# Performance work log

Measured on AMD Instinct MI355X. Metric: run time of the kernel, lower is better.

## Reference

```python
import jax, jax.numpy as jnp
import numpy as np

B, S, D, H = 4, 2048, 1024, 16
HD = D // H  # head size = 64


def setup_inputs() -> dict:
    key = jax.random.key(0)
    ks = jax.random.split(key, 5)
    x = jax.random.normal(ks[0], (B, S, D), dtype=jnp.float32)
    scale = 1.0 / np.sqrt(D)
    Wq = jax.random.normal(ks[1], (H, D, HD), dtype=jnp.float32) * scale
    Wk = jax.random.normal(ks[2], (H, D, HD), dtype=jnp.float32) * scale
    Wv = jax.random.normal(ks[3], (H, D, HD), dtype=jnp.float32) * scale
    W_O = jax.random.normal(ks[4], (D, D), dtype=jnp.float32) * scale
    return {"x": x, "Wq": Wq, "Wk": Wk, "Wv": Wv, "W_O": W_O}


def reference(x, Wq, Wk, Wv, W_O):
    # Per-head Q/K/V projections, batched across heads via einsum.
    q = jnp.einsum("bsd,hde->bhse", x, Wq)  # [B,H,S,HD]
    k = jnp.einsum("bsd,hde->bhse", x, Wk)
    v = jnp.einsum("bsd,hde->bhse", x, Wv)
    scores = jnp.einsum("bhse,bhte->bhst", q, k) / jnp.sqrt(
        jnp.asarray(HD, dtype=x.dtype)
    )  # [B,H,S,S]
    # Causal mask (GPT-style attention head).
    causal = jnp.tril(jnp.ones((S, S), dtype=bool))
    scores = jnp.where(causal, scores, jnp.finfo(scores.dtype).min)
    attn = jax.nn.softmax(scores, axis=-1)
    out = jnp.einsum("bhst,bhte->bhse", attn, v)  # [B,H,S,HD]
    # Concat heads: [B,S,H,HD] -> [B,S,D]
    concat = out.transpose(0, 2, 1, 3).reshape(B, S, D)
    # nn.Linear(D, D, bias=False): y = x @ W_O^T
    return concat @ W_O.T
```

## Files before the change

### kernel.cpp

```cpp
#include <hip/hip_runtime.h>
#include <hip/hip_bf16.h>

#define BB 4
#define SS 2048
#define DD 1024
#define HH 16
#define HDD 64

typedef __attribute__((ext_vector_type(8))) short bf16x8;
typedef __attribute__((ext_vector_type(8))) unsigned short u16x8;
typedef __attribute__((ext_vector_type(4))) float f32x4;
typedef __attribute__((ext_vector_type(4))) unsigned int u32x4;

#define GLD_LDS16(g, l) \
    __builtin_amdgcn_global_load_lds((const __attribute__((address_space(1))) void*)(g), \
                                     (__attribute__((address_space(3))) void*)(l), 16, 0, 0)

__device__ __forceinline__ unsigned short f32_to_bf16(float f) {
    unsigned int u = __float_as_uint(f);
    u += 0x7fffu + ((u >> 16) & 1u);
    return (unsigned short)(u >> 16);
}

__device__ __forceinline__ unsigned int cvt_pk_bf16(float lo, float hi) {
    unsigned int r;
    asm("v_cvt_pk_bf16_f32 %0, %1, %2" : "=v"(r) : "v"(lo), "v"(hi));
    return r;
}

__global__ __launch_bounds__(256) void prep(
    const float* __restrict__ x, const float* __restrict__ Wq,
    const float* __restrict__ Wk, const float* __restrict__ Wv,
    const float* __restrict__ WO, unsigned short* __restrict__ xb,
    unsigned short* __restrict__ wob, unsigned short* __restrict__ wqkvT) {
    __shared__ float tile[64][68];
    int bid = blockIdx.x, t = threadIdx.x;
    if (bid < 2048) {
        for (int i = bid * 256 + t; i < 2097152; i += 2048 * 256) {
            float4 v = ((const float4*)x)[i];
            ushort4 o;
            o.x = f32_to_bf16(v.x); o.y = f32_to_bf16(v.y);
            o.z = f32_to_bf16(v.z); o.w = f32_to_bf16(v.w);
            ((ushort4*)xb)[i] = o;
        }
    } else if (bid < 2304) {
        for (int i = (bid - 2048) * 256 + t; i < 262144; i += 256 * 256) {
            float4 v = ((const float4*)WO)[i];
            ushort4 o;
            o.x = f32_to_bf16(v.x); o.y = f32_to_bf16(v.y);
            o.z = f32_to_bf16(v.z); o.w = f32_to_bf16(v.w);
            ((ushort4*)wob)[i] = o;
        }
    } else {
        int b2 = bid - 2304;
        int w = b2 >> 8, h = (b2 >> 4) & 15, db = b2 & 15;
        const float* src = (w == 0) ? Wq : ((w == 1) ? Wk : Wv);
        for (int p = t; p < 1024; p += 256) {
            int row = p >> 4, c4 = p & 15;
            float4 v = *(const float4*)(src + ((size_t)(h * 1024 + db * 64 + row)) * 64 + c4 * 4);
            tile[row][c4 * 4 + 0] = v.x; tile[row][c4 * 4 + 1] = v.y;
            tile[row][c4 * 4 + 2] = v.z; tile[row][c4 * 4 + 3] = v.w;
        }
        __syncthreads();
        size_t wbase = (size_t)w * 1024 * 1024;
        for (int p = t; p < 512; p += 256) {
            int e = p >> 3, c = p & 7;
            u16x8 pk;
#pragma unroll
            for (int j = 0; j < 8; ++j) pk[j] = f32_to_bf16(tile[c * 8 + j][e]);
            *(u16x8*)(wqkvT + wbase + (size_t)(h * 64 + e) * 1024 + db * 64 + c * 8) = pk;
        }
    }
}

template <int EPI>
__global__ __launch_bounds__(256) void gemm128(
    const unsigned short* __restrict__ A, const unsigned short* __restrict__ Bm,
    void* __restrict__ C0, void* __restrict__ C1, void* __restrict__ C2, int NBt) {
    __shared__ unsigned short sh[2][128 * 64];
    int cpx = gridDim.x >> 3;
    int bid = (blockIdx.x & 7) * cpx + (blockIdx.x >> 3);
    int mb = bid / NBt, nb = bid % NBt;
    int tid = threadIdx.x;
    int lane = tid & 63, wid = tid >> 6;
    int wm = wid >> 1, wn = wid & 1;
    int g = lane >> 4, lr = lane & 15;
    int srow = lane >> 3, sch = lane & 7;
    int scol = (sch ^ srow) * 8;
    const int M0 = mb * 128, N0 = nb * 128;

    f32x4 acc[4][4] = {};

    for (int kt = 0; kt < 16; ++kt) {
        __syncthreads();
#pragma unroll
        for (int i = 0; i < 4; ++i) {
            int c = wid * 4 + i;
            int row = c * 8 + srow;
            GLD_LDS16(A + (size_t)(M0 + row) * 1024 + kt * 64 + scol, &sh[0][c * 512]);
            GLD_LDS16(Bm + (size_t)(N0 + row) * 1024 + kt * 64 + scol, &sh[1][c * 512]);
        }
        __syncthreads();
#pragma unroll
        for (int kk = 0; kk < 2; ++kk) {
            bf16x8 af[4], bfr[4];
#pragma unroll
            for (int i = 0; i < 4; ++i) {
                int row = wm * 64 + i * 16 + lr;
                int ch = (kk * 4 + g) ^ (row & 7);
                af[i] = *(const bf16x8*)&sh[0][row * 64 + ch * 8];
                int rowb = wn * 64 + i * 16 + lr;
                int chb = (kk * 4 + g) ^ (rowb & 7);
                bfr[i] = *(const bf16x8*)&sh[1][rowb * 64 + chb * 8];
            }
            __builtin_amdgcn_s_setprio(1);
#pragma unroll
            for (int i = 0; i < 4; ++i)
#pragma unroll
                for (int j = 0; j < 4; ++j)
                    acc[i][j] = __builtin_amdgcn_mfma_f32_16x16x32_bf16(af[i], bfr[j], acc[i][j], 0, 0, 0);
            __builtin_amdgcn_s_setprio(0);
        }
    }

    if constexpr (EPI == 0) {
        unsigned short (*T)[128] = (unsigned short(*)[128])sh;
        if (nb < 16) {
            unsigned short* dst0 = (nb < 8) ? (unsigned short*)C0 : (unsigned short*)C1;
            const float QSCALE = 0.125f * 1.4426950408889634f;
            float scl = (nb < 8) ? QSCALE : 1.0f;
            __syncthreads();
#pragma unroll
            for (int i = 0; i < 4; ++i)
#pragma unroll
                for (int j = 0; j < 4; ++j)
#pragma unroll
                    for (int r = 0; r < 4; ++r) {
                        int ml = wm * 64 + i * 16 + g * 4 + r;
                        int nl = wn * 64 + j * 16 + lr;
                        T[ml][nl ^ ((ml & 7) << 3)] = f32_to_bf16(acc[i][j][r] * scl);
                    }
            __syncthreads();
            int b = M0 >> 11, s0 = M0 & 2047;
            int h0 = (N0 >> 6) & 15;
#pragma unroll
            for (int itr = 0; itr < 8; ++itr) {
                int idx = itr * 256 + tid;
                int row = idx >> 4, seg = idx & 15;
                u16x8 vv = *(const u16x8*)&T[row][(seg * 8) ^ ((row & 7) << 3)];
                int h = h0 + (seg >> 3), e0 = (seg & 7) * 8;
                *(u16x8*)(dst0 + ((size_t)(b * HH + h) * SS + s0 + row) * HDD + e0) = vv;
            }
        } else {
            __syncthreads();
#pragma unroll
            for (int i = 0; i < 4; ++i)
#pragma unroll
                for (int j = 0; j < 4; ++j)
#pragma unroll
                    for (int r = 0; r < 4; ++r) {
                        int nl = wn * 64 + j * 16 + lr;
                        int ml = wm * 64 + i * 16 + g * 4 + r;
                        T[nl][ml ^ ((nl & 7) << 3)] = f32_to_bf16(acc[i][j][r]);
                    }
            __syncthreads();
            unsigned short* Vo = (unsigned short*)C2;
            int b = M0 >> 11, s0 = M0 & 2047;
            int nb16 = nb - 16;
#pragma unroll
            for (int itr = 0; itr < 8; ++itr) {
                int idx = itr * 256 + tid;
                int row = idx >> 4, seg = idx & 15;
                u16x8 vv = *(const u16x8*)&T[row][(seg * 8) ^ ((row & 7) << 3)];
                int h = (nb16 * 128 + row) >> 6;
                int e = row & 63;
                *(u16x8*)(Vo + (((size_t)(b * HH + h)) * HDD + e) * SS + s0 + seg * 8) = vv;
            }
        }
    } else {
        float* Co = (float*)C0;
#pragma unroll
        for (int i = 0; i < 4; ++i)
#pragma unroll
            for (int j = 0; j < 4; ++j)
#pragma unroll
                for (int r = 0; r < 4; ++r) {
                    int m = M0 + wm * 64 + i * 16 + g * 4 + r;
                    int n = N0 + wn * 64 + j * 16 + lr;
                    Co[(size_t)m * 1024 + n] = acc[i][j][r];
                }
    }
}

__global__ __launch_bounds__(256, 4) void attn_fwd(
    const unsigned short* __restrict__ Q, const unsigned short* __restrict__ K,
    const unsigned short* __restrict__ VT, unsigned short* __restrict__ O) {
    int bid = blockIdx.x;
    int qb = 15 - (bid >> 6);
    int bh = bid & 63;
    int b = bh >> 4, h = bh & 15;
    int tid = threadIdx.x, lane = tid & 63, w = tid >> 6;
    int g = lane >> 4, lr = lane & 15;
    int srow = lane >> 3, sch = lane & 7;
    int scol = (sch ^ srow) * 8;

    __shared__ unsigned short smem[16384];

    const int q0 = qb * 128;
    const unsigned short* Qp = Q + ((size_t)bh * SS + q0 + w * 32) * HDD;
    const unsigned short* Kp = K + (size_t)bh * SS * HDD;
    const unsigned short* Vp = VT + (size_t)bh * HDD * SS;

    bf16x8 qf[2][2];
#pragma unroll
    for (int qg = 0; qg < 2; ++qg) {
        qf[qg][0] = *(const bf16x8*)(Qp + (qg * 16 + lr) * 64 + g * 8);
        qf[qg][1] = *(const bf16x8*)(Qp + (qg * 16 + lr) * 64 + 32 + g * 8);
    }

    bf16x8 ones;
#pragma unroll
    for (int i = 0; i < 8; ++i) ones[i] = (short)0x3F80;

    f32x4 acc[2][4] = {};
    f32x4 acc_l[2] = {};

    const int nt = 2 * qb + 2;

#pragma unroll
    for (int i = 0; i < 2; ++i) {
        int c = w * 2 + i;
        int row = c * 8 + srow;
        GLD_LDS16(Kp + (size_t)row * HDD + scol, smem + c * 512);
        GLD_LDS16(Vp + (size_t)row * SS + scol, smem + 8192 + c * 512);
    }
    __syncthreads();

    auto tile_body = [&](int it, unsigned short* Kcur, unsigned short* Vcur,
                         unsigned short* Knxt, unsigned short* Vnxt, bool stage) {
        if (stage) {
            int t1 = (it + 1) * 64;
#pragma unroll
            for (int i = 0; i < 2; ++i) {
                int c = w * 2 + i;
                int row = c * 8 + srow;
                GLD_LDS16(Kp + (size_t)(t1 + row) * HDD + scol, Knxt + c * 512);
                GLD_LDS16(Vp + (size_t)row * SS + t1 + scol, Vnxt + c * 512);
            }
        }
        int t0 = it * 64;

        f32x4 sacc[2][4] = {};
        __builtin_amdgcn_s_setprio(1);
#pragma unroll
        for (int kk = 0; kk < 2; ++kk)
#pragma unroll
            for (int ct = 0; ct < 4; ++ct) {
                int row = ct * 16 + lr;
                int ch = (kk * 4 + g) ^ (row & 7);
                bf16x8 kf = *(const bf16x8*)(Kcur + row * 64 + ch * 8);
#pragma unroll
                for (int qg = 0; qg < 2; ++qg)
                    sacc[qg][ct] = __builtin_amdgcn_mfma_f32_16x16x32_bf16(kf, qf[qg][kk], sacc[qg][ct], 0, 0, 0);
            }
        __builtin_amdgcn_s_setprio(0);

        if (it >= nt - 2) {
#pragma unroll
            for (int qg = 0; qg < 2; ++qg) {
                int kmax = q0 + w * 32 + qg * 16 + lr - t0;
#pragma unroll
                for (int ct = 0; ct < 4; ++ct)
#pragma unroll
                    for (int r = 0; r < 4; ++r)
                        if (ct * 16 + g * 4 + r > kmax) sacc[qg][ct][r] = -3.0e38f;
            }
        }

        bf16x8 pvf[2][2];
#pragma unroll
        for (int qg = 0; qg < 2; ++qg) {
            unsigned int pk[4][2];
#pragma unroll
            for (int ct = 0; ct < 4; ++ct) {
                float p0 = exp2f(sacc[qg][ct][0]);
                float p1 = exp2f(sacc[qg][ct][1]);
                float p2 = exp2f(sacc[qg][ct][2]);
                float p3 = exp2f(sacc[qg][ct][3]);
                pk[ct][0] = cvt_pk_bf16(p0, p1);
                pk[ct][1] = cvt_pk_bf16(p2, p3);
            }
            unsigned int out[2][4];
#pragma unroll
            for (int s5 = 0; s5 < 2; ++s5)
#pragma unroll
                for (int s1 = 0; s1 < 2; ++s1) {
                    unsigned int a = pk[2 * s5][s1];
                    unsigned int bq = pk[2 * s5 + 1][s1];
                    asm("v_permlane32_swap_b32 %0, %1" : "+v"(a), "+v"(bq));
                    asm("v_permlane16_swap_b32 %0, %1" : "+v"(a), "+v"(bq));
                    out[s5][s1] = a;
                    out[s5][2 + s1] = bq;
                }
#pragma unroll
            for (int kk2 = 0; kk2 < 2; ++kk2) {
                u32x4 tmp;
                tmp[0] = out[kk2][0]; tmp[1] = out[kk2][1];
                tmp[2] = out[kk2][2]; tmp[3] = out[kk2][3];
                pvf[qg][kk2] = __builtin_bit_cast(bf16x8, tmp);
            }
#pragma unroll
            for (int kk2 = 0; kk2 < 2; ++kk2)
                acc_l[qg] = __builtin_amdgcn_mfma_f32_16x16x32_bf16(ones, pvf[qg][kk2], acc_l[qg], 0, 0, 0);
        }

        __builtin_amdgcn_s_setprio(1);
#pragma unroll
        for (int kk2 = 0; kk2 < 2; ++kk2)
#pragma unroll
            for (int ct2 = 0; ct2 < 4; ++ct2) {
                int row = ct2 * 16 + lr;
                int ch = (kk2 * 4 + g) ^ (row & 7);
                bf16x8 vf = *(const bf16x8*)(Vcur + row * 64 + ch * 8);
#pragma unroll
                for (int qg = 0; qg < 2; ++qg)
                    acc[qg][ct2] = __builtin_amdgcn_mfma_f32_16x16x32_bf16(vf, pvf[qg][kk2], acc[qg][ct2], 0, 0, 0);
            }
        __builtin_amdgcn_s_setprio(0);

        __syncthreads();
    };

    for (int it = 0; it < nt; it += 2) {
        tile_body(it,     smem,        smem + 8192,  smem + 4096, smem + 12288, true);
        tile_body(it + 1, smem + 4096, smem + 12288, smem,        smem + 8192,  it + 2 < nt);
    }

#pragma unroll
    for (int qg = 0; qg < 2; ++qg) {
        float invl = 1.0f / acc_l[qg][0];
#pragma unroll
        for (int ct2 = 0; ct2 < 4; ++ct2)
#pragma unroll
            for (int r = 0; r < 4; ++r)
                smem[(w * 32 + qg * 16 + lr) * 72 + ct2 * 16 + g * 4 + r] =
                    f32_to_bf16(acc[qg][ct2][r] * invl);
    }
    __syncthreads();
#pragma unroll
    for (int itr = 0; itr < 4; ++itr) {
        int idx = itr * 256 + tid;
        int row = idx >> 3, seg = idx & 7;
        u16x8 vv = *(const u16x8*)&smem[row * 72 + seg * 8];
        *(u16x8*)(O + ((size_t)(b * SS + q0 + row)) * DD + h * 64 + seg * 8) = vv;
    }
}

extern "C" void kernel_launch(void* const* d_in, const int* in_sizes, int n_in,
                              void* d_out, int out_size, void* d_ws, size_t ws_size,
                              hipStream_t stream) {
    (void)in_sizes; (void)n_in; (void)out_size; (void)ws_size;
    const float* x  = (const float*)d_in[0];
    const float* Wq = (const float*)d_in[1];
    const float* Wk = (const float*)d_in[2];
    const float* Wv = (const float*)d_in[3];
    const float* WO = (const float*)d_in[4];
    float* out = (float*)d_out;

    char* ws = (char*)d_ws;
    unsigned short* xb    = (unsigned short*)(ws + 0);
    unsigned short* wqkvT = (unsigned short*)(ws + 16777216);
    unsigned short* wob   = (unsigned short*)(ws + 23068672);
    unsigned short* Qb    = (unsigned short*)(ws + 25165824);
    unsigned short* Kb    = (unsigned short*)(ws + 41943040);
    unsigned short* VTb   = (unsigned short*)(ws + 75497472);
    unsigned short* Ob    = (unsigned short*)(ws + 92274688);

    prep<<<3072, 256, 0, stream>>>(x, Wq, Wk, Wv, WO, xb, wob, wqkvT);
    gemm128<0><<<64 * 24, 256, 0, stream>>>(xb, wqkvT, (void*)Qb, (void*)Kb, (void*)VTb, 24);
    attn_fwd<<<1024, 256, 0, stream>>>(Qb, Kb, VTb, Ob);
    gemm128<1><<<64 * 8, 256, 0, stream>>>(Ob, wob, (void*)out, nullptr, nullptr, 8);
}
```

Measured before the change: 162.7 us.

## Widen attention blocks to 256 query rows with 8 waves sharing K/V tiles

After: 178.2 us. 1.1x slower.

```diff
diff --git a/kernel.cpp b/kernel.cpp
--- a/kernel.cpp
+++ b/kernel.cpp
@@ -192,11 +192,12 @@
     }
 }
 
-__global__ __launch_bounds__(256, 4) void attn_fwd(
+__global__ __launch_bounds__(512) void attn_fwd(
     const unsigned short* __restrict__ Q, const unsigned short* __restrict__ K,
     const unsigned short* __restrict__ VT, unsigned short* __restrict__ O) {
     int bid = blockIdx.x;
-    int qb = 15 - (bid >> 6);
+    int xg = bid >> 6;
+    int qb = (xg < 4) ? (7 - xg) : (xg - 4);
     int bh = bid & 63;
     int b = bh >> 4, h = bh & 15;
     int tid = threadIdx.x, lane = tid & 63, w = tid >> 6;
@@ -206,7 +207,7 @@
 
     __shared__ unsigned short smem[16384];
 
-    const int q0 = qb * 128;
+    const int q0 = qb * 256;
     const unsigned short* Qp = Q + ((size_t)bh * SS + q0 + w * 32) * HDD;
     const unsigned short* Kp = K + (size_t)bh * SS * HDD;
     const unsigned short* Vp = VT + (size_t)bh * HDD * SS;
@@ -225,14 +226,12 @@
     f32x4 acc[2][4] = {};
     f32x4 acc_l[2] = {};
 
-    const int nt = 2 * qb + 2;
-
-#pragma unroll
-    for (int i = 0; i < 2; ++i) {
-        int c = w * 2 + i;
-        int row = c * 8 + srow;
-        GLD_LDS16(Kp + (size_t)row * HDD + scol, smem + c * 512);
-        GLD_LDS16(Vp + (size_t)row * SS + scol, smem + 8192 + c * 512);
+    const int nt = 4 * qb + 4;
+
+    {
+        int row = w * 8 + srow;
+        GLD_LDS16(Kp + (size_t)row * HDD + scol, smem + w * 512);
+        GLD_LDS16(Vp + (size_t)row * SS + scol, smem + 8192 + w * 512);
     }
     __syncthreads();
 
@@ -240,13 +239,9 @@
                          unsigned short* Knxt, unsigned short* Vnxt, bool stage) {
         if (stage) {
             int t1 = (it + 1) * 64;
-#pragma unroll
-            for (int i = 0; i < 2; ++i) {
-                int c = w * 2 + i;
-                int row = c * 8 + srow;
-                GLD_LDS16(Kp + (size_t)(t1 + row) * HDD + scol, Knxt + c * 512);
-                GLD_LDS16(Vp + (size_t)row * SS + t1 + scol, Vnxt + c * 512);
-            }
+            int row = w * 8 + srow;
+            GLD_LDS16(Kp + (size_t)(t1 + row) * HDD + scol, Knxt + w * 512);
+            GLD_LDS16(Vp + (size_t)row * SS + t1 + scol, Vnxt + w * 512);
         }
         int t0 = it * 64;
 
@@ -265,7 +260,7 @@
             }
         __builtin_amdgcn_s_setprio(0);
 
-        if (it >= nt - 2) {
+        if (it >= nt - 4) {
 #pragma unroll
             for (int qg = 0; qg < 2; ++qg) {
                 int kmax = q0 + w * 32 + qg * 16 + lr - t0;
@@ -336,23 +331,28 @@
         tile_body(it + 1, smem + 4096, smem + 12288, smem,        smem + 8192,  it + 2 < nt);
     }
 
-#pragma unroll
-    for (int qg = 0; qg < 2; ++qg) {
-        float invl = 1.0f / acc_l[qg][0];
-#pragma unroll
-        for (int ct2 = 0; ct2 < 4; ++ct2)
-#pragma unroll
-            for (int r = 0; r < 4; ++r)
-                smem[(w * 32 + qg * 16 + lr) * 72 + ct2 * 16 + g * 4 + r] =
-                    f32_to_bf16(acc[qg][ct2][r] * invl);
-    }
-    __syncthreads();
-#pragma unroll
-    for (int itr = 0; itr < 4; ++itr) {
-        int idx = itr * 256 + tid;
-        int row = idx >> 3, seg = idx & 7;
-        u16x8 vv = *(const u16x8*)&smem[row * 72 + seg * 8];
-        *(u16x8*)(O + ((size_t)(b * SS + q0 + row)) * DD + h * 64 + seg * 8) = vv;
+    float invl[2] = {1.0f / acc_l[0][0], 1.0f / acc_l[1][0]};
+#pragma unroll
+    for (int hv = 0; hv < 2; ++hv) {
+        if ((w >> 2) == hv) {
+#pragma unroll
+            for (int qg = 0; qg < 2; ++qg)
+#pragma unroll
+                for (int ct2 = 0; ct2 < 4; ++ct2)
+#pragma unroll
+                    for (int r = 0; r < 4; ++r)
+                        smem[((w & 3) * 32 + qg * 16 + lr) * 72 + ct2 * 16 + g * 4 + r] =
+                            f32_to_bf16(acc[qg][ct2][r] * invl[qg]);
+        }
+        __syncthreads();
+#pragma unroll
+        for (int itr = 0; itr < 2; ++itr) {
+            int idx = itr * 512 + tid;
+            int row = idx >> 3, seg = idx & 7;
+            u16x8 vv = *(const u16x8*)&smem[row * 72 + seg * 8];
+            *(u16x8*)(O + ((size_t)(b * SS + q0 + hv * 128 + row)) * DD + h * 64 + seg * 8) = vv;
+        }
+        __syncthreads();
     }
 }
 
@@ -378,6 +378,6 @@
 
     prep<<<3072, 256, 0, stream>>>(x, Wq, Wk, Wv, WO, xb, wob, wqkvT);
     gemm128<0><<<64 * 24, 256, 0, stream>>>(xb, wqkvT, (void*)Qb, (void*)Kb, (void*)VTb, 24);
-    attn_fwd<<<1024, 256, 0, stream>>>(Qb, Kb, VTb, Ob);
+    attn_fwd<<<512, 512, 0, stream>>>(Qb, Kb, VTb, Ob);
     gemm128<1><<<64 * 8, 256, 0, stream>>>(Ob, wob, (void*)out, nullptr, nullptr, 8);
 }
```
